# Kernel optimization log

Measured on AMD Instinct MI355X. Metric: run time of the kernel, lower is better.

Reference implementation:

```python
import jax, jax.numpy as jnp
import numpy as np
from jax import lax

V = 128     # vocab_size
E = 512     # embed_size
H = 1024    # hidden_size
NE = 10     # num_experts
B = 32
S = 1024


def setup_inputs() -> dict:
    key = jax.random.key(0)
    ks = jax.random.split(key, 11)
    s = 0.05
    return {
        "x": jax.random.randint(ks[0], (B, S), 0, V),
        "emb": jax.random.normal(ks[1], (V, E), jnp.float32) * s,
        "W_ih": jax.random.normal(ks[2], (4 * H, E), jnp.float32) * s,   # gates i,f,g,o
        "W_hh": jax.random.normal(ks[3], (4 * H, H), jnp.float32) * s,
        "b_ih": jax.random.normal(ks[4], (4 * H,), jnp.float32) * s,
        "b_hh": jax.random.normal(ks[5], (4 * H,), jnp.float32) * s,
        "We": jax.random.normal(ks[6], (NE, V, H), jnp.float32) * s,    # expert Linear weights
        "be": jax.random.normal(ks[7], (NE, V), jnp.float32) * s,
        "Wg": jax.random.normal(ks[8], (NE, H), jnp.float32) * s,       # gating Linear
        "bg": jax.random.normal(ks[9], (NE,), jnp.float32) * s,
    }


def _lstm(xe, W_ih, W_hh, b_ih, b_hh):
    # xe: [B,S,E] -> hidden states [B,S,H]; PyTorch LSTM gate order i,f,g,o
    pre = jnp.einsum("bse,ge->bsg", xe, W_ih) + b_ih  # [B,S,4H], input proj hoisted out of scan
    h0 = jnp.zeros((xe.shape[0], H), xe.dtype)
    c0 = jnp.zeros((xe.shape[0], H), xe.dtype)

    def step(carry, p):
        h, c = carry
        g = p + h @ W_hh.T + b_hh
        i, f, gg, o = jnp.split(g, 4, axis=-1)
        c = jax.nn.sigmoid(f) * c + jax.nn.sigmoid(i) * jnp.tanh(gg)
        h = jax.nn.sigmoid(o) * jnp.tanh(c)
        return (h, c), h

    _, hs = lax.scan(step, (h0, c0), pre.transpose(1, 0, 2))  # scan over S
    return hs.transpose(1, 0, 2)  # [B,S,H]


def reference(x, emb, W_ih, W_hh, b_ih, b_hh, We, be, Wg, bg):
    xe = emb[x]                                   # [B,S,E]
    h = _lstm(xe, W_ih, W_hh, b_ih, b_hh)         # [B,S,H]
    # all experts as one batched GEMM: [NE,B,S,V]
    expert_outputs = jnp.einsum("bsh,evh->ebsv", h, We) + be[:, None, None, :]
    gating_weights = jax.nn.softmax(h[:, -1, :] @ Wg.T + bg, axis=-1)  # [B,NE]
    combined = jnp.einsum("be,ebsv->bsv", gating_weights, expert_outputs)
    return combined, expert_outputs, gating_weights
```

## Files before the change

kernel.cpp:

```cpp
#include <hip/hip_runtime.h>
#include <hip/hip_bf16.h>
#include <math.h>

#define V_  128
#define E_  512
#define H_  1024
#define NE_ 10
#define B_  32
#define S_  1024
#define G4H (4*H_)

typedef short bf16x8 __attribute__((ext_vector_type(8)));
typedef float f32x4  __attribute__((ext_vector_type(4)));

__device__ __forceinline__ short f2bf(float f) {
    __hip_bfloat16 h = __float2bfloat16(f);
    short s; __builtin_memcpy(&s, &h, 2); return s;
}
__device__ __forceinline__ float bf2f(ushort u) {
    unsigned int x = ((unsigned int)u) << 16;
    float f; __builtin_memcpy(&f, &x, 4); return f;
}
__device__ __forceinline__ float sigf(float x) { return 1.f / (1.f + __expf(-x)); }
__device__ __forceinline__ float tanhfast(float x) { return 1.f - 2.f / (__expf(2.f * x) + 1.f); }

__device__ __forceinline__ int4 gload4_sc(const void* p) {
    int4 r;
    asm volatile("global_load_dwordx4 %0, %1, off sc0 sc1" : "=&v"(r) : "v"(p));
    return r;
}
__device__ __forceinline__ int gload1_sc(const void* p) {
    int r;
    asm volatile("global_load_dword %0, %1, off sc0 sc1" : "=&v"(r) : "v"(p));
    return r;
}
__device__ __forceinline__ void gstore2_sc(void* p, int2 v) {
    asm volatile("global_store_dwordx2 %0, %1, off sc0 sc1" :: "v"(p), "v"(v) : "memory");
}
__device__ __forceinline__ void gstore1_sc(void* p, int v) {
    asm volatile("global_store_dword %0, %1, off sc0 sc1" :: "v"(p), "v"(v) : "memory");
}
#define WAITCNT0() do { asm volatile("s_waitcnt vmcnt(0)" ::: "memory"); \
                        __builtin_amdgcn_sched_barrier(0); } while (0)

__global__ __launch_bounds__(256) void build_T(
    const float* __restrict__ emb, const float* __restrict__ W_ih,
    const float* __restrict__ b_ih, float* __restrict__ T2)
{
    int idx = blockIdx.x * 256 + threadIdx.x;
    int g = idx >> 7, v = idx & 127;
    const float* er = emb + v * E_;
    const float* wr = W_ih + (size_t)g * E_;
    float acc = b_ih[g];
    #pragma unroll 4
    for (int e = 0; e < E_; ++e) acc += er[e] * wr[e];
    T2[v * G4H + (g & 1023) * 4 + (g >> 10)] = acc;
}

__global__ __launch_bounds__(256) void conv_bf16(
    const float* __restrict__ src, ushort* __restrict__ dst, int n)
{
    int i = blockIdx.x * 256 + threadIdx.x;
    if (i < n) dst[i] = (ushort)f2bf(src[i]);
}

__global__ __launch_bounds__(512) void lstm_scan(
    const int* __restrict__ x, const float* __restrict__ T2,
    const float* __restrict__ W_hh, const float* __restrict__ b_hh,
    ushort* __restrict__ hbuf, ushort* __restrict__ h_all, int* __restrict__ flags)
{
    const int p = blockIdx.x, tid = threadIdx.x;
    const int lane = tid & 63, wave = tid >> 6;
    const int m = lane & 15, kg = lane >> 4;
    const int kslice = wave & 3, chalf = wave >> 2;
    const int k0 = kslice * 256;

    __shared__ float part_lds[8 * 256];
    __shared__ float pre_s[32][17];
    __shared__ float bhh_l[16];

    bf16x8 afrag[8];
    {
        const float* wbase = W_hh + (size_t)((m & 3) * H_ + p * 4 + (m >> 2)) * H_;
        #pragma unroll
        for (int kk = 0; kk < 8; ++kk) {
            int kb = k0 + kk * 32 + kg * 8;
            float4 w0 = *(const float4*)(wbase + kb);
            float4 w1 = *(const float4*)(wbase + kb + 4);
            bf16x8 a;
            a[0]=f2bf(w0.x); a[1]=f2bf(w0.y); a[2]=f2bf(w0.z); a[3]=f2bf(w0.w);
            a[4]=f2bf(w1.x); a[5]=f2bf(w1.y); a[6]=f2bf(w1.z); a[7]=f2bf(w1.w);
            afrag[kk] = a;
        }
    }
    if (tid < 16) bhh_l[tid] = b_hh[(tid & 3) * H_ + p * 4 + (tid >> 2)];

    int boff[8];
    #pragma unroll
    for (int kk = 0; kk < 8; ++kk)
        boff[kk] = (chalf * 16 + m) * H_ + k0 + kk * 32 + kg * 8;

    const int bb = lane >> 1, u0 = (lane & 1) * 2;
    float c0 = 0.f, c1 = 0.f;

    ushort* hb0 = hbuf;
    ushort* hb1 = hbuf + B_ * H_;
    __syncthreads();

    for (int t = 0; t < S_; ++t) {
        const ushort* hrd = (t & 1) ? hb0 : hb1;
        ushort*       hwr = (t & 1) ? hb1 : hb0;

        {
            const int src = kslice * 64 + lane;
            for (;;) {
                int f = gload1_sc(flags + src * 16);
                WAITCNT0();
                if (__all(f >= t)) break;
                __builtin_amdgcn_s_sleep(1);
            }
        }

        int4 braw[8];
        #pragma unroll
        for (int i = 0; i < 8; ++i) braw[i] = gload4_sc(hrd + boff[i]);
        WAITCNT0();
        f32x4 accA = {0.f,0.f,0.f,0.f}, accB = {0.f,0.f,0.f,0.f};
        #pragma unroll
        for (int kk = 0; kk < 4; ++kk) {
            bf16x8 b0, b1;
            __builtin_memcpy(&b0, &braw[kk * 2],     16);
            __builtin_memcpy(&b1, &braw[kk * 2 + 1], 16);
            accA = __builtin_amdgcn_mfma_f32_16x16x32_bf16(afrag[kk * 2],     b0, accA, 0, 0, 0);
            accB = __builtin_amdgcn_mfma_f32_16x16x32_bf16(afrag[kk * 2 + 1], b1, accB, 0, 0, 0);
        }
        #pragma unroll
        for (int d = 0; d < 4; ++d)
            part_lds[wave * 256 + (kg * 4 + d) * 16 + m] = accA[d] + accB[d];
        __syncthreads();

        {
            int c2 = tid >> 8, idx = tid & 255;
            float s = part_lds[(c2 * 4 + 0) * 256 + idx] + part_lds[(c2 * 4 + 1) * 256 + idx]
                    + part_lds[(c2 * 4 + 2) * 256 + idx] + part_lds[(c2 * 4 + 3) * 256 + idx];
            pre_s[c2 * 16 + (idx & 15)][idx >> 4] = s;
        }
        __syncthreads();

        if (wave == 0) {
            int xv = x[bb * S_ + t];
            const float* Tv = T2 + (size_t)xv * G4H + (size_t)(p * 4 + u0) * 4;
            float4 ga = *(const float4*)Tv;
            float4 gb = *(const float4*)(Tv + 4);
            int r0 = u0 * 4, r1 = r0 + 4;
            float pi0 = pre_s[bb][r0+0] + ga.x + bhh_l[r0+0];
            float pf0 = pre_s[bb][r0+1] + ga.y + bhh_l[r0+1];
            float pg0 = pre_s[bb][r0+2] + ga.z + bhh_l[r0+2];
            float po0 = pre_s[bb][r0+3] + ga.w + bhh_l[r0+3];
            float pi1 = pre_s[bb][r1+0] + gb.x + bhh_l[r1+0];
            float pf1 = pre_s[bb][r1+1] + gb.y + bhh_l[r1+1];
            float pg1 = pre_s[bb][r1+2] + gb.z + bhh_l[r1+2];
            float po1 = pre_s[bb][r1+3] + gb.w + bhh_l[r1+3];
            c0 = sigf(pf0) * c0 + sigf(pi0) * tanhfast(pg0);
            c1 = sigf(pf1) * c1 + sigf(pi1) * tanhfast(pg1);
            float h0 = sigf(po0) * tanhfast(c0);
            float h1 = sigf(po1) * tanhfast(c1);

            unsigned int hp = (unsigned int)(unsigned short)f2bf(h0)
                            | ((unsigned int)(unsigned short)f2bf(h1) << 16);
            *(unsigned int*)(h_all + (size_t)bb * (S_ * H_) + (size_t)t * H_ + (p * 4 + u0)) = hp;

            unsigned int hq = __shfl_xor((int)hp, 1);
            if (!(lane & 1)) {
                int2 hv; hv.x = (int)hp; hv.y = (int)hq;
                gstore2_sc(hwr + bb * H_ + p * 4, hv);
            }
            asm volatile("s_waitcnt vmcnt(0)" ::: "memory");
            if (lane == 0) gstore1_sc(flags + p * 16, t + 1);
        }
    }
}

__global__ __launch_bounds__(256) void expert_gemm(
    const ushort* __restrict__ A, const ushort* __restrict__ Bw,
    const float* __restrict__ be, float* __restrict__ out)
{
    __shared__ ushort As[128][40];
    __shared__ ushort Bs[128][40];
    const int tid = threadIdx.x;
    const int bm = blockIdx.x / 10, bn = blockIdx.x % 10;
    const int m0 = bm * 128, n0 = bn * 128;
    const int lane = tid & 63, wave = tid >> 6;
    const int wm = wave >> 1, wn = wave & 1;
    const int fm = lane & 15, kg = lane >> 4;

    const int srow = tid >> 1, scol = (tid & 1) * 16;
    const ushort* Ag = A  + (size_t)(m0 + srow) * H_ + scol;
    const ushort* Bg = Bw + (size_t)(n0 + srow) * H_ + scol;

    f32x4 acc[4][4];
    #pragma unroll
    for (int i = 0; i < 4; ++i)
        #pragma unroll
        for (int j = 0; j < 4; ++j) acc[i][j] = (f32x4){0.f,0.f,0.f,0.f};

    int4 ra0 = *(const int4*)(Ag),     ra1 = *(const int4*)(Ag + 8);
    int4 rb0 = *(const int4*)(Bg),     rb1 = *(const int4*)(Bg + 8);

    for (int k0 = 0; k0 < H_; k0 += 32) {
        __syncthreads();
        *(int4*)&As[srow][scol] = ra0;  *(int4*)&As[srow][scol + 8] = ra1;
        *(int4*)&Bs[srow][scol] = rb0;  *(int4*)&Bs[srow][scol + 8] = rb1;
        __syncthreads();
        if (k0 + 32 < H_) {
            ra0 = *(const int4*)(Ag + k0 + 32);  ra1 = *(const int4*)(Ag + k0 + 40);
            rb0 = *(const int4*)(Bg + k0 + 32);  rb1 = *(const int4*)(Bg + k0 + 40);
        }
        bf16x8 af[4], bf[4];
        #pragma unroll
        for (int i = 0; i < 4; ++i) af[i] = *(const bf16x8*)&As[wm * 64 + i * 16 + fm][kg * 8];
        #pragma unroll
        for (int j = 0; j < 4; ++j) bf[j] = *(const bf16x8*)&Bs[wn * 64 + j * 16 + fm][kg * 8];
        #pragma unroll
        for (int i = 0; i < 4; ++i)
            #pragma unroll
            for (int j = 0; j < 4; ++j)
                acc[i][j] = __builtin_amdgcn_mfma_f32_16x16x32_bf16(af[i], bf[j], acc[i][j], 0, 0, 0);
    }

    const int e = bn;
    const size_t ebase = (size_t)e * ((size_t)B_ * S_ * V_);
    #pragma unroll
    for (int i = 0; i < 4; ++i) {
        #pragma unroll
        for (int d = 0; d < 4; ++d) {
            int row = m0 + wm * 64 + i * 16 + kg * 4 + d;
            float* orow = out + ebase + (size_t)row * V_;
            #pragma unroll
            for (int j = 0; j < 4; ++j) {
                int col = wn * 64 + j * 16 + fm;
                orow[col] = acc[i][j][d] + be[n0 + col];
            }
        }
    }
}

__global__ __launch_bounds__(256) void gating_kernel(
    const ushort* __restrict__ h_all, const float* __restrict__ Wg,
    const float* __restrict__ bg, float* __restrict__ gate_out)
{
    int b = blockIdx.x;
    int tid = threadIdx.x;
    __shared__ float red[NE_][256];
    const ushort* h = h_all + (size_t)b * (S_ * H_) + (size_t)(S_ - 1) * H_;
    float pa[NE_];
    #pragma unroll
    for (int e = 0; e < NE_; ++e) pa[e] = 0.f;
    for (int k = tid; k < H_; k += 256) {
        float hv = bf2f(h[k]);
        #pragma unroll
        for (int e = 0; e < NE_; ++e) pa[e] += hv * Wg[e * H_ + k];
    }
    #pragma unroll
    for (int e = 0; e < NE_; ++e) red[e][tid] = pa[e];
    __syncthreads();
    for (int s = 128; s > 0; s >>= 1) {
        if (tid < s) {
            #pragma unroll
            for (int e = 0; e < NE_; ++e) red[e][tid] += red[e][tid + s];
        }
        __syncthreads();
    }
    if (tid == 0) {
        float lg[NE_], mx = -1e30f;
        #pragma unroll
        for (int e = 0; e < NE_; ++e) { lg[e] = red[e][0] + bg[e]; mx = fmaxf(mx, lg[e]); }
        float s = 0.f;
        #pragma unroll
        for (int e = 0; e < NE_; ++e) { lg[e] = expf(lg[e] - mx); s += lg[e]; }
        #pragma unroll
        for (int e = 0; e < NE_; ++e) gate_out[b * NE_ + e] = lg[e] / s;
    }
}

__global__ __launch_bounds__(256) void combine_kernel(
    const float* __restrict__ exp_out, const float* __restrict__ gate,
    float* __restrict__ comb)
{
    int idx = blockIdx.x * 256 + threadIdx.x;
    int b = idx >> 17;
    float acc = 0.f;
    #pragma unroll
    for (int e = 0; e < NE_; ++e)
        acc += gate[b * NE_ + e] * exp_out[(size_t)e * (size_t)(B_ * S_ * V_) + idx];
    comb[idx] = acc;
}

extern "C" void kernel_launch(void* const* d_in, const int* in_sizes, int n_in,
                              void* d_out, int out_size, void* d_ws, size_t ws_size,
                              hipStream_t stream)
{
    const int*   x    = (const int*)  d_in[0];
    const float* emb  = (const float*)d_in[1];
    const float* W_ih = (const float*)d_in[2];
    const float* W_hh = (const float*)d_in[3];
    const float* b_ih = (const float*)d_in[4];
    const float* b_hh = (const float*)d_in[5];
    const float* We   = (const float*)d_in[6];
    const float* be   = (const float*)d_in[7];
    const float* Wg   = (const float*)d_in[8];
    const float* bg   = (const float*)d_in[9];

    float* out     = (float*)d_out;
    float* comb    = out;
    float* exp_out = out + 4194304;
    float* gate    = out + 4194304 + 41943040;

    char*   ws    = (char*)d_ws;
    float*  T2    = (float*)ws;
    ushort* hbuf  = (ushort*)(ws + (2u << 20));
    int*    flags = (int*)   (ws + (2u << 20) + (128u << 10));
    ushort* We_bf = (ushort*)(ws + (4u << 20));
    ushort* h_all = (ushort*)(ws + (8u << 20));

    hipMemsetAsync(ws + (2u << 20), 0, (144u << 10), stream);

    build_T      <<<2048, 256, 0, stream>>>(emb, W_ih, b_ih, T2);
    conv_bf16    <<<(NE_ * V_ * H_ + 255) / 256, 256, 0, stream>>>(We, We_bf, NE_ * V_ * H_);
    lstm_scan    <<<256, 512, 0, stream>>>(x, T2, W_hh, b_hh, hbuf, h_all, flags);
    expert_gemm  <<<256 * 10, 256, 0, stream>>>(h_all, We_bf, be, exp_out);
    gating_kernel<<<B_, 256, 0, stream>>>(h_all, Wg, bg, gate);
    combine_kernel<<<4194304 / 256, 256, 0, stream>>>(exp_out, gate, comb);
}
```

Before: 5.483 ms.

## Replace per-step flag barrier with step-tagged hidden-state words in LSTM scan

The cross-block sync in the persistent LSTM scan no longer uses separate flag words. Each bf16 hidden value is now stored in a 32-bit word with the step number in the upper 16 bits, and readers spin on the data itself until every tag matches. This drops the flag poll, the store-then-wait-then-flag serialization, and one round trip per timestep. In exchange each step moves twice as many bytes of hidden state and spends extra ALU work checking tags and repacking the words into bf16 fragments.

```diff
diff --git a/kernel.cpp b/kernel.cpp
--- a/kernel.cpp
+++ b/kernel.cpp
@@ -12,6 +12,7 @@
 
 typedef short bf16x8 __attribute__((ext_vector_type(8)));
 typedef float f32x4  __attribute__((ext_vector_type(4)));
+typedef int   i32x4  __attribute__((ext_vector_type(4)));
 
 __device__ __forceinline__ short f2bf(float f) {
     __hip_bfloat16 h = __float2bfloat16(f);
@@ -24,21 +25,13 @@
 __device__ __forceinline__ float sigf(float x) { return 1.f / (1.f + __expf(-x)); }
 __device__ __forceinline__ float tanhfast(float x) { return 1.f - 2.f / (__expf(2.f * x) + 1.f); }
 
-__device__ __forceinline__ int4 gload4_sc(const void* p) {
-    int4 r;
+__device__ __forceinline__ i32x4 gload4_sc(const void* p) {
+    i32x4 r;
     asm volatile("global_load_dwordx4 %0, %1, off sc0 sc1" : "=&v"(r) : "v"(p));
     return r;
 }
-__device__ __forceinline__ int gload1_sc(const void* p) {
-    int r;
-    asm volatile("global_load_dword %0, %1, off sc0 sc1" : "=&v"(r) : "v"(p));
-    return r;
-}
-__device__ __forceinline__ void gstore2_sc(void* p, int2 v) {
-    asm volatile("global_store_dwordx2 %0, %1, off sc0 sc1" :: "v"(p), "v"(v) : "memory");
-}
-__device__ __forceinline__ void gstore1_sc(void* p, int v) {
-    asm volatile("global_store_dword %0, %1, off sc0 sc1" :: "v"(p), "v"(v) : "memory");
+__device__ __forceinline__ void gstore4_sc(void* p, i32x4 v) {
+    asm volatile("global_store_dwordx4 %0, %1, off sc0 sc1" :: "v"(p), "v"(v) : "memory");
 }
 #define WAITCNT0() do { asm volatile("s_waitcnt vmcnt(0)" ::: "memory"); \
                         __builtin_amdgcn_sched_barrier(0); } while (0)
@@ -67,7 +60,7 @@
 __global__ __launch_bounds__(512) void lstm_scan(
     const int* __restrict__ x, const float* __restrict__ T2,
     const float* __restrict__ W_hh, const float* __restrict__ b_hh,
-    ushort* __restrict__ hbuf, ushort* __restrict__ h_all, int* __restrict__ flags)
+    unsigned int* __restrict__ tagbuf, ushort* __restrict__ h_all)
 {
     const int p = blockIdx.x, tid = threadIdx.x;
     const int lane = tid & 63, wave = tid >> 6;
@@ -98,39 +91,55 @@
     int boff[8];
     #pragma unroll
     for (int kk = 0; kk < 8; ++kk)
-        boff[kk] = (chalf * 16 + m) * H_ + k0 + kk * 32 + kg * 8;
+        boff[kk] = (chalf * 16 + m) * 1024 + k0 + kk * 32 + kg * 8;
 
     const int bb = lane >> 1, u0 = (lane & 1) * 2;
     float c0 = 0.f, c1 = 0.f;
 
-    ushort* hb0 = hbuf;
-    ushort* hb1 = hbuf + B_ * H_;
+    unsigned int* tb0 = tagbuf;
+    unsigned int* tb1 = tagbuf + 32 * 1024;
     __syncthreads();
 
     for (int t = 0; t < S_; ++t) {
-        const ushort* hrd = (t & 1) ? hb0 : hb1;
-        ushort*       hwr = (t & 1) ? hb1 : hb0;
-
-        {
-            const int src = kslice * 64 + lane;
-            for (;;) {
-                int f = gload1_sc(flags + src * 16);
-                WAITCNT0();
-                if (__all(f >= t)) break;
-                __builtin_amdgcn_s_sleep(1);
+        const unsigned int* trd = (t & 1) ? tb0 : tb1;
+        unsigned int*       twr = (t & 1) ? tb1 : tb0;
+
+        i32x4 braw[16];
+        const unsigned int exp_tag = (unsigned int)t;
+        for (;;) {
+            #pragma unroll
+            for (int kk = 0; kk < 8; ++kk) {
+                braw[kk * 2]     = gload4_sc(trd + boff[kk]);
+                braw[kk * 2 + 1] = gload4_sc(trd + boff[kk] + 4);
             }
-        }
-
-        int4 braw[8];
-        #pragma unroll
-        for (int i = 0; i < 8; ++i) braw[i] = gload4_sc(hrd + boff[i]);
-        WAITCNT0();
+            WAITCNT0();
+            unsigned int bad = 0;
+            #pragma unroll
+            for (int i = 0; i < 16; ++i)
+                #pragma unroll
+                for (int d = 0; d < 4; ++d)
+                    bad |= (((unsigned int)braw[i][d]) >> 16) ^ exp_tag;
+            if (__all(bad == 0)) break;
+            __builtin_amdgcn_s_sleep(1);
+        }
+
         f32x4 accA = {0.f,0.f,0.f,0.f}, accB = {0.f,0.f,0.f,0.f};
         #pragma unroll
         for (int kk = 0; kk < 4; ++kk) {
+            i32x4 loA = braw[(kk * 2) * 2],     hiA = braw[(kk * 2) * 2 + 1];
+            i32x4 loB = braw[(kk * 2 + 1) * 2], hiB = braw[(kk * 2 + 1) * 2 + 1];
+            i32x4 fa, fb;
+            fa[0] = (loA[0] & 0xFFFF) | (loA[1] << 16);
+            fa[1] = (loA[2] & 0xFFFF) | (loA[3] << 16);
+            fa[2] = (hiA[0] & 0xFFFF) | (hiA[1] << 16);
+            fa[3] = (hiA[2] & 0xFFFF) | (hiA[3] << 16);
+            fb[0] = (loB[0] & 0xFFFF) | (loB[1] << 16);
+            fb[1] = (loB[2] & 0xFFFF) | (loB[3] << 16);
+            fb[2] = (hiB[0] & 0xFFFF) | (hiB[1] << 16);
+            fb[3] = (hiB[2] & 0xFFFF) | (hiB[3] << 16);
             bf16x8 b0, b1;
-            __builtin_memcpy(&b0, &braw[kk * 2],     16);
-            __builtin_memcpy(&b1, &braw[kk * 2 + 1], 16);
+            __builtin_memcpy(&b0, &fa, 16);
+            __builtin_memcpy(&b1, &fb, 16);
             accA = __builtin_amdgcn_mfma_f32_16x16x32_bf16(afrag[kk * 2],     b0, accA, 0, 0, 0);
             accB = __builtin_amdgcn_mfma_f32_16x16x32_bf16(afrag[kk * 2 + 1], b1, accB, 0, 0, 0);
         }
@@ -166,17 +175,22 @@
             float h0 = sigf(po0) * tanhfast(c0);
             float h1 = sigf(po1) * tanhfast(c1);
 
-            unsigned int hp = (unsigned int)(unsigned short)f2bf(h0)
-                            | ((unsigned int)(unsigned short)f2bf(h1) << 16);
-            *(unsigned int*)(h_all + (size_t)bb * (S_ * H_) + (size_t)t * H_ + (p * 4 + u0)) = hp;
-
-            unsigned int hq = __shfl_xor((int)hp, 1);
-            if (!(lane & 1)) {
-                int2 hv; hv.x = (int)hp; hv.y = (int)hq;
-                gstore2_sc(hwr + bb * H_ + p * 4, hv);
+            unsigned int b0 = (unsigned int)(unsigned short)f2bf(h0);
+            unsigned int b1 = (unsigned int)(unsigned short)f2bf(h1);
+            *(unsigned int*)(h_all + (size_t)bb * (S_ * H_) + (size_t)t * H_ + (p * 4 + u0))
+                = b0 | (b1 << 16);
+
+            if (t < S_ - 1) {
+                unsigned int tg = ((unsigned int)(t + 1)) << 16;
+                unsigned int d0 = b0 | tg;
+                unsigned int d1 = b1 | tg;
+                unsigned int e0 = (unsigned int)__shfl_xor((int)d0, 1);
+                unsigned int e1 = (unsigned int)__shfl_xor((int)d1, 1);
+                if (!(lane & 1)) {
+                    i32x4 v; v[0] = (int)d0; v[1] = (int)d1; v[2] = (int)e0; v[3] = (int)e1;
+                    gstore4_sc(twr + bb * 1024 + p * 4, v);
+                }
             }
-            asm volatile("s_waitcnt vmcnt(0)" ::: "memory");
-            if (lane == 0) gstore1_sc(flags + p * 16, t + 1);
         }
     }
 }
@@ -216,16 +230,16 @@
             ra0 = *(const int4*)(Ag + k0 + 32);  ra1 = *(const int4*)(Ag + k0 + 40);
             rb0 = *(const int4*)(Bg + k0 + 32);  rb1 = *(const int4*)(Bg + k0 + 40);
         }
-        bf16x8 af[4], bf[4];
+        bf16x8 af[4], bfv[4];
         #pragma unroll
         for (int i = 0; i < 4; ++i) af[i] = *(const bf16x8*)&As[wm * 64 + i * 16 + fm][kg * 8];
         #pragma unroll
-        for (int j = 0; j < 4; ++j) bf[j] = *(const bf16x8*)&Bs[wn * 64 + j * 16 + fm][kg * 8];
+        for (int j = 0; j < 4; ++j) bfv[j] = *(const bf16x8*)&Bs[wn * 64 + j * 16 + fm][kg * 8];
         #pragma unroll
         for (int i = 0; i < 4; ++i)
             #pragma unroll
             for (int j = 0; j < 4; ++j)
-                acc[i][j] = __builtin_amdgcn_mfma_f32_16x16x32_bf16(af[i], bf[j], acc[i][j], 0, 0, 0);
+                acc[i][j] = __builtin_amdgcn_mfma_f32_16x16x32_bf16(af[i], bfv[j], acc[i][j], 0, 0, 0);
     }
 
     const int e = bn;
@@ -316,18 +330,17 @@
     float* exp_out = out + 4194304;
     float* gate    = out + 4194304 + 41943040;
 
-    char*   ws    = (char*)d_ws;
-    float*  T2    = (float*)ws;
-    ushort* hbuf  = (ushort*)(ws + (2u << 20));
-    int*    flags = (int*)   (ws + (2u << 20) + (128u << 10));
-    ushort* We_bf = (ushort*)(ws + (4u << 20));
-    ushort* h_all = (ushort*)(ws + (8u << 20));
-
-    hipMemsetAsync(ws + (2u << 20), 0, (144u << 10), stream);
+    char*         ws     = (char*)d_ws;
+    float*        T2     = (float*)ws;
+    unsigned int* tagbuf = (unsigned int*)(ws + (2u << 20));
+    ushort*       We_bf  = (ushort*)(ws + (4u << 20));
+    ushort*       h_all  = (ushort*)(ws + (8u << 20));
+
+    (void)hipMemsetAsync(ws + (2u << 20), 0, (256u << 10), stream);
 
     build_T      <<<2048, 256, 0, stream>>>(emb, W_ih, b_ih, T2);
     conv_bf16    <<<(NE_ * V_ * H_ + 255) / 256, 256, 0, stream>>>(We, We_bf, NE_ * V_ * H_);
-    lstm_scan    <<<256, 512, 0, stream>>>(x, T2, W_hh, b_hh, hbuf, h_all, flags);
+    lstm_scan    <<<256, 512, 0, stream>>>(x, T2, W_hh, b_hh, tagbuf, h_all);
     expert_gemm  <<<256 * 10, 256, 0, stream>>>(h_all, We_bf, be, exp_out);
     gating_kernel<<<B_, 256, 0, stream>>>(h_all, Wg, bg, gate);
     combine_kernel<<<4194304 / 256, 256, 0, stream>>>(exp_out, gate, comb);
```

Result: slower. 16.30 ms (+197.3%).

## Halve LSTM scan blocks, keep W_hh slice in LDS, widen h exchange

Applied to the files above, without the earlier changes.

The persistent LSTM scan now runs on 128 blocks instead of 256, each owning 8 hidden units (32 gate rows). Its bf16 W_hh slice is stored in a swizzled 64KB LDS array instead of register fragments. All 512 threads compute gates in parallel and stage h through LDS, so one wave publishes it with 16-byte stores. Cache-control bits drop sc0, which makes flag polling and h loads cheaper. Fewer blocks mean fewer flag readers per step and less cross-block synchronisation, at the cost of more MFMA and LDS work per block on the serial critical path.

```diff
diff --git a/kernel.cpp b/kernel.cpp
--- a/kernel.cpp
+++ b/kernel.cpp
@@ -12,6 +12,7 @@
 
 typedef short bf16x8 __attribute__((ext_vector_type(8)));
 typedef float f32x4  __attribute__((ext_vector_type(4)));
+typedef int   i32x4  __attribute__((ext_vector_type(4)));
 
 __device__ __forceinline__ short f2bf(float f) {
     __hip_bfloat16 h = __float2bfloat16(f);
@@ -24,21 +25,16 @@
 __device__ __forceinline__ float sigf(float x) { return 1.f / (1.f + __expf(-x)); }
 __device__ __forceinline__ float tanhfast(float x) { return 1.f - 2.f / (__expf(2.f * x) + 1.f); }
 
-__device__ __forceinline__ int4 gload4_sc(const void* p) {
-    int4 r;
-    asm volatile("global_load_dwordx4 %0, %1, off sc0 sc1" : "=&v"(r) : "v"(p));
+__device__ __forceinline__ i32x4 gload4_sc(const void* p) {
+    i32x4 r;
+    asm volatile("global_load_dwordx4 %0, %1, off sc1" : "=&v"(r) : "v"(p));
     return r;
 }
-__device__ __forceinline__ int gload1_sc(const void* p) {
-    int r;
-    asm volatile("global_load_dword %0, %1, off sc0 sc1" : "=&v"(r) : "v"(p));
-    return r;
-}
-__device__ __forceinline__ void gstore2_sc(void* p, int2 v) {
-    asm volatile("global_store_dwordx2 %0, %1, off sc0 sc1" :: "v"(p), "v"(v) : "memory");
+__device__ __forceinline__ void gstore4_sc(void* p, i32x4 v) {
+    asm volatile("global_store_dwordx4 %0, %1, off sc1" :: "v"(p), "v"(v) : "memory");
 }
 __device__ __forceinline__ void gstore1_sc(void* p, int v) {
-    asm volatile("global_store_dword %0, %1, off sc0 sc1" :: "v"(p), "v"(v) : "memory");
+    asm volatile("global_store_dword %0, %1, off sc1" :: "v"(p), "v"(v) : "memory");
 }
 #define WAITCNT0() do { asm volatile("s_waitcnt vmcnt(0)" ::: "memory"); \
                         __builtin_amdgcn_sched_barrier(0); } while (0)
@@ -69,42 +65,42 @@
     const float* __restrict__ W_hh, const float* __restrict__ b_hh,
     ushort* __restrict__ hbuf, ushort* __restrict__ h_all, int* __restrict__ flags)
 {
-    const int p = blockIdx.x, tid = threadIdx.x;
+    const int p = blockIdx.x;
+    const int tid = threadIdx.x;
     const int lane = tid & 63, wave = tid >> 6;
     const int m = lane & 15, kg = lane >> 4;
-    const int kslice = wave & 3, chalf = wave >> 2;
-    const int k0 = kslice * 256;
-
-    __shared__ float part_lds[8 * 256];
-    __shared__ float pre_s[32][17];
-    __shared__ float bhh_l[16];
-
-    bf16x8 afrag[8];
-    {
-        const float* wbase = W_hh + (size_t)((m & 3) * H_ + p * 4 + (m >> 2)) * H_;
-        #pragma unroll
-        for (int kk = 0; kk < 8; ++kk) {
-            int kb = k0 + kk * 32 + kg * 8;
-            float4 w0 = *(const float4*)(wbase + kb);
-            float4 w1 = *(const float4*)(wbase + kb + 4);
-            bf16x8 a;
-            a[0]=f2bf(w0.x); a[1]=f2bf(w0.y); a[2]=f2bf(w0.z); a[3]=f2bf(w0.w);
-            a[4]=f2bf(w1.x); a[5]=f2bf(w1.y); a[6]=f2bf(w1.z); a[7]=f2bf(w1.w);
-            afrag[kk] = a;
-        }
-    }
-    if (tid < 16) bhh_l[tid] = b_hh[(tid & 3) * H_ + p * 4 + (tid >> 2)];
+    const int bh = wave & 1, kq = wave >> 1;
+
+    __shared__ __align__(16) ushort Wl[32 * 1024];
+    __shared__ float  part[8 * 512];
+    __shared__ __align__(16) float pre_s[32][36];
+    __shared__ __align__(16) ushort hstage[256];
+    __shared__ float  bhh_l[32];
+
+    #pragma unroll
+    for (int i = 0; i < 8; ++i) {
+        int grp = tid + i * 512;
+        int r = grp >> 7, k8 = (grp & 127) * 8;
+        const float* wsrc = W_hh + (size_t)((r & 3) * H_ + p * 8 + (r >> 2)) * H_ + k8;
+        float4 w0 = *(const float4*)wsrc;
+        float4 w1 = *(const float4*)(wsrc + 4);
+        bf16x8 a;
+        a[0]=f2bf(w0.x); a[1]=f2bf(w0.y); a[2]=f2bf(w0.z); a[3]=f2bf(w0.w);
+        a[4]=f2bf(w1.x); a[5]=f2bf(w1.y); a[6]=f2bf(w1.z); a[7]=f2bf(w1.w);
+        *(bf16x8*)&Wl[r * 1024 + (k8 ^ ((r & 7) << 3))] = a;
+    }
+    if (tid < 32) bhh_l[tid] = b_hh[(tid & 3) * H_ + p * 8 + (tid >> 2)];
 
     int boff[8];
     #pragma unroll
     for (int kk = 0; kk < 8; ++kk)
-        boff[kk] = (chalf * 16 + m) * H_ + k0 + kk * 32 + kg * 8;
-
-    const int bb = lane >> 1, u0 = (lane & 1) * 2;
-    float c0 = 0.f, c1 = 0.f;
-
+        boff[kk] = (bh * 16 + m) * 1024 + kq * 256 + kk * 32 + kg * 8;
+
+    const int eb = tid >> 3, eu = tid & 7;
+    float cst = 0.f;
     ushort* hb0 = hbuf;
     ushort* hb1 = hbuf + B_ * H_;
+    const int swz = (m & 7) << 3;
     __syncthreads();
 
     for (int t = 0; t < S_; ++t) {
@@ -112,68 +108,79 @@
         ushort*       hwr = (t & 1) ? hb1 : hb0;
 
         {
-            const int src = kslice * 64 + lane;
+            const int src = kq * 32 + (lane & 31);
+            const int* fp = flags + src * 16;
             for (;;) {
-                int f = gload1_sc(flags + src * 16);
-                WAITCNT0();
+                int f;
+                asm volatile("global_load_dword %0, %1, off sc1\n\ts_waitcnt vmcnt(0)"
+                             : "=&v"(f) : "v"(fp) : "memory");
+                __builtin_amdgcn_sched_barrier(0);
                 if (__all(f >= t)) break;
                 __builtin_amdgcn_s_sleep(1);
             }
         }
 
-        int4 braw[8];
-        #pragma unroll
-        for (int i = 0; i < 8; ++i) braw[i] = gload4_sc(hrd + boff[i]);
+        i32x4 braw[8];
+        #pragma unroll
+        for (int kk = 0; kk < 8; ++kk) braw[kk] = gload4_sc(hrd + boff[kk]);
         WAITCNT0();
-        f32x4 accA = {0.f,0.f,0.f,0.f}, accB = {0.f,0.f,0.f,0.f};
-        #pragma unroll
-        for (int kk = 0; kk < 4; ++kk) {
-            bf16x8 b0, b1;
-            __builtin_memcpy(&b0, &braw[kk * 2],     16);
-            __builtin_memcpy(&b1, &braw[kk * 2 + 1], 16);
-            accA = __builtin_amdgcn_mfma_f32_16x16x32_bf16(afrag[kk * 2],     b0, accA, 0, 0, 0);
-            accB = __builtin_amdgcn_mfma_f32_16x16x32_bf16(afrag[kk * 2 + 1], b1, accB, 0, 0, 0);
-        }
-        #pragma unroll
-        for (int d = 0; d < 4; ++d)
-            part_lds[wave * 256 + (kg * 4 + d) * 16 + m] = accA[d] + accB[d];
-        __syncthreads();
-
+
+        f32x4 acc0 = {0.f,0.f,0.f,0.f}, acc1 = {0.f,0.f,0.f,0.f};
+        #pragma unroll
+        for (int kk = 0; kk < 8; ++kk) {
+            int koff = (kq * 256 + kk * 32 + kg * 8) ^ swz;
+            bf16x8 a0 = *(const bf16x8*)&Wl[m * 1024 + koff];
+            bf16x8 a1 = *(const bf16x8*)&Wl[(16 + m) * 1024 + koff];
+            bf16x8 bv; __builtin_memcpy(&bv, &braw[kk], 16);
+            acc0 = __builtin_amdgcn_mfma_f32_16x16x32_bf16(a0, bv, acc0, 0, 0, 0);
+            acc1 = __builtin_amdgcn_mfma_f32_16x16x32_bf16(a1, bv, acc1, 0, 0, 0);
+        }
         {
-            int c2 = tid >> 8, idx = tid & 255;
-            float s = part_lds[(c2 * 4 + 0) * 256 + idx] + part_lds[(c2 * 4 + 1) * 256 + idx]
-                    + part_lds[(c2 * 4 + 2) * 256 + idx] + part_lds[(c2 * 4 + 3) * 256 + idx];
-            pre_s[c2 * 16 + (idx & 15)][idx >> 4] = s;
-        }
-        __syncthreads();
+            float* pw = part + wave * 512;
+            #pragma unroll
+            for (int d = 0; d < 4; ++d) {
+                pw[(kg * 4 + d) * 16 + m]       = acc0[d];
+                pw[256 + (kg * 4 + d) * 16 + m] = acc1[d];
+            }
+        }
+        __syncthreads();
+
+        #pragma unroll
+        for (int i = 0; i < 2; ++i) {
+            int flat = tid + i * 512;
+            float s = part[flat] + part[1024 + flat] + part[2048 + flat] + part[3072 + flat];
+            int b = ((flat >> 9) & 1) * 16 + (flat & 15);
+            int r = ((flat >> 8) & 1) * 16 + ((flat >> 4) & 15);
+            pre_s[b][r] = s;
+        }
+        __syncthreads();
+
+        if (tid < 256) {
+            int xv = x[eb * S_ + t];
+            float4 tv = *(const float4*)(T2 + (size_t)xv * G4H + (size_t)(p * 8 + eu) * 4);
+            float4 pv = *(const float4*)&pre_s[eb][eu * 4];
+            int r0 = eu * 4;
+            float pi = pv.x + tv.x + bhh_l[r0 + 0];
+            float pf = pv.y + tv.y + bhh_l[r0 + 1];
+            float pg = pv.z + tv.z + bhh_l[r0 + 2];
+            float po = pv.w + tv.w + bhh_l[r0 + 3];
+            cst = sigf(pf) * cst + sigf(pi) * tanhfast(pg);
+            float h = sigf(po) * tanhfast(cst);
+            unsigned int hb16 = (unsigned int)(unsigned short)f2bf(h);
+            unsigned int hn = (unsigned int)__shfl_xor((int)hb16, 1);
+            if (!(eu & 1))
+                *(unsigned int*)(h_all + (size_t)eb * (S_ * H_) + (size_t)t * H_ + (p * 8 + eu))
+                    = hb16 | (hn << 16);
+            hstage[tid] = (ushort)hb16;
+        }
+        __syncthreads();
+
+        if (t == S_ - 1) break;
 
         if (wave == 0) {
-            int xv = x[bb * S_ + t];
-            const float* Tv = T2 + (size_t)xv * G4H + (size_t)(p * 4 + u0) * 4;
-            float4 ga = *(const float4*)Tv;
-            float4 gb = *(const float4*)(Tv + 4);
-            int r0 = u0 * 4, r1 = r0 + 4;
-            float pi0 = pre_s[bb][r0+0] + ga.x + bhh_l[r0+0];
-            float pf0 = pre_s[bb][r0+1] + ga.y + bhh_l[r0+1];
-            float pg0 = pre_s[bb][r0+2] + ga.z + bhh_l[r0+2];
-            float po0 = pre_s[bb][r0+3] + ga.w + bhh_l[r0+3];
-            float pi1 = pre_s[bb][r1+0] + gb.x + bhh_l[r1+0];
-            float pf1 = pre_s[bb][r1+1] + gb.y + bhh_l[r1+1];
-            float pg1 = pre_s[bb][r1+2] + gb.z + bhh_l[r1+2];
-            float po1 = pre_s[bb][r1+3] + gb.w + bhh_l[r1+3];
-            c0 = sigf(pf0) * c0 + sigf(pi0) * tanhfast(pg0);
-            c1 = sigf(pf1) * c1 + sigf(pi1) * tanhfast(pg1);
-            float h0 = sigf(po0) * tanhfast(c0);
-            float h1 = sigf(po1) * tanhfast(c1);
-
-            unsigned int hp = (unsigned int)(unsigned short)f2bf(h0)
-                            | ((unsigned int)(unsigned short)f2bf(h1) << 16);
-            *(unsigned int*)(h_all + (size_t)bb * (S_ * H_) + (size_t)t * H_ + (p * 4 + u0)) = hp;
-
-            unsigned int hq = __shfl_xor((int)hp, 1);
-            if (!(lane & 1)) {
-                int2 hv; hv.x = (int)hp; hv.y = (int)hq;
-                gstore2_sc(hwr + bb * H_ + p * 4, hv);
+            if (lane < 32) {
+                i32x4 v = *(const i32x4*)&hstage[lane * 8];
+                gstore4_sc(hwr + lane * 1024 + p * 8, v);
             }
             asm volatile("s_waitcnt vmcnt(0)" ::: "memory");
             if (lane == 0) gstore1_sc(flags + p * 16, t + 1);
@@ -216,16 +223,16 @@
             ra0 = *(const int4*)(Ag + k0 + 32);  ra1 = *(const int4*)(Ag + k0 + 40);
             rb0 = *(const int4*)(Bg + k0 + 32);  rb1 = *(const int4*)(Bg + k0 + 40);
         }
-        bf16x8 af[4], bf[4];
+        bf16x8 af[4], bfv[4];
         #pragma unroll
         for (int i = 0; i < 4; ++i) af[i] = *(const bf16x8*)&As[wm * 64 + i * 16 + fm][kg * 8];
         #pragma unroll
-        for (int j = 0; j < 4; ++j) bf[j] = *(const bf16x8*)&Bs[wn * 64 + j * 16 + fm][kg * 8];
+        for (int j = 0; j < 4; ++j) bfv[j] = *(const bf16x8*)&Bs[wn * 64 + j * 16 + fm][kg * 8];
         #pragma unroll
         for (int i = 0; i < 4; ++i)
             #pragma unroll
             for (int j = 0; j < 4; ++j)
-                acc[i][j] = __builtin_amdgcn_mfma_f32_16x16x32_bf16(af[i], bf[j], acc[i][j], 0, 0, 0);
+                acc[i][j] = __builtin_amdgcn_mfma_f32_16x16x32_bf16(af[i], bfv[j], acc[i][j], 0, 0, 0);
     }
 
     const int e = bn;
@@ -323,11 +330,11 @@
     ushort* We_bf = (ushort*)(ws + (4u << 20));
     ushort* h_all = (ushort*)(ws + (8u << 20));
 
-    hipMemsetAsync(ws + (2u << 20), 0, (144u << 10), stream);
+    (void)hipMemsetAsync(ws + (2u << 20), 0, (136u << 10), stream);
 
     build_T      <<<2048, 256, 0, stream>>>(emb, W_ih, b_ih, T2);
     conv_bf16    <<<(NE_ * V_ * H_ + 255) / 256, 256, 0, stream>>>(We, We_bf, NE_ * V_ * H_);
-    lstm_scan    <<<256, 512, 0, stream>>>(x, T2, W_hh, b_hh, hbuf, h_all, flags);
+    lstm_scan    <<<128, 512, 0, stream>>>(x, T2, W_hh, b_hh, hbuf, h_all, flags);
     expert_gemm  <<<256 * 10, 256, 0, stream>>>(h_all, We_bf, be, exp_out);
     gating_kernel<<<B_, 256, 0, stream>>>(h_all, Wg, bg, gate);
     combine_kernel<<<4194304 / 256, 256, 0, stream>>>(exp_out, gate, comb);
```

Measured after the change: 4.985 ms (median of 2 runs). -9.1%, faster.
